# Kernel tuning notes

Measured on AMD Instinct MI355X. Metric: run time of the kernel, lower is better.

Reference implementation:

```python
import jax, jax.numpy as jnp
import numpy as np

DIM = 768
NUM_HEADS = 12
HIDDEN = int(DIM * 4.0)
EPS = 1e-5


def setup_inputs() -> dict:
    key = jax.random.key(0)
    ks = jax.random.split(key, 8)
    s = lambda k, shape, scale=0.02: jax.random.normal(k, shape, dtype=jnp.float32) * scale
    return {
        "x": jax.random.normal(ks[0], (8, 1024, DIM), dtype=jnp.float32),
        "ln1_g": jnp.ones((DIM,), jnp.float32),
        "ln1_b": jnp.zeros((DIM,), jnp.float32),
        "qkv_w": s(ks[1], (DIM, 3 * DIM)),
        "qkv_b": jnp.zeros((3 * DIM,), jnp.float32),
        "proj_w": s(ks[2], (DIM, DIM)),
        "proj_b": jnp.zeros((DIM,), jnp.float32),
        "ln2_g": jnp.ones((DIM,), jnp.float32),
        "ln2_b": jnp.zeros((DIM,), jnp.float32),
        "fc1_w": s(ks[3], (DIM, HIDDEN)),
        "fc1_b": jnp.zeros((HIDDEN,), jnp.float32),
        "fc2_w": s(ks[4], (HIDDEN, DIM)),
        "fc2_b": jnp.zeros((DIM,), jnp.float32),
    }


def layer_norm(x, g, b):
    mu = jnp.mean(x, axis=-1, keepdims=True)
    var = jnp.mean(jnp.square(x - mu), axis=-1, keepdims=True)
    return (x - mu) * jax.lax.rsqrt(var + EPS) * g + b


def reference(x, ln1_g, ln1_b, qkv_w, qkv_b, proj_w, proj_b,
              ln2_g, ln2_b, fc1_w, fc1_b, fc2_w, fc2_b):
    B, N, C = x.shape
    H = NUM_HEADS
    Dh = C // H
    scale = Dh ** -0.5

    # --- Attention (pre-norm) ---
    h = layer_norm(x, ln1_g, ln1_b)
    qkv = h @ qkv_w + qkv_b                       # [B, N, 3C]
    qkv = qkv.reshape(B, N, 3, H, Dh)
    q, k, v = qkv[:, :, 0], qkv[:, :, 1], qkv[:, :, 2]  # [B, N, H, Dh]
    attn = jnp.einsum("bqhd,bkhd->bhqk", q, k) * scale  # [B, H, N, N]
    attn = jax.nn.softmax(attn, axis=-1)
    o = jnp.einsum("bhqk,bkhd->bqhd", attn, v).reshape(B, N, C)
    x = x + (o @ proj_w + proj_b)

    # --- MLP (pre-norm) ---
    h = layer_norm(x, ln2_g, ln2_b)
    h = jax.nn.gelu(h @ fc1_w + fc1_b, approximate=False)  # torch nn.GELU = exact erf
    x = x + (h @ fc2_w + fc2_b)
    return x
```

## Files before the change

kernel.cpp:

```cpp
#include <hip/hip_runtime.h>
#include <hip/hip_bf16.h>
#include <cstdint>

using f32x4   = __attribute__((ext_vector_type(4))) float;
using f32x16  = __attribute__((ext_vector_type(16))) float;
using bf16x8  = __attribute__((ext_vector_type(8))) short;

__device__ inline ushort f2bf(float f) {
    union { float f; uint u; } x; x.f = f;
    uint u = x.u;
    return (ushort)((u + 0x7FFFu + ((u >> 16) & 1u)) >> 16);
}

__device__ inline void gload16(const ushort* g, ushort* lds) {
    __builtin_amdgcn_global_load_lds(
        (const __attribute__((address_space(1))) unsigned int*)g,
        (__attribute__((address_space(3))) unsigned int*)lds, 16, 0, 0);
}

__global__ __launch_bounds__(256) void transpose_cast(const float* __restrict__ w,
                                                      ushort* __restrict__ wt,
                                                      int K, int N) {
    __shared__ float tile[32][33];
    const int bn = blockIdx.x * 32;
    const int bk = blockIdx.y * 32;
    const int tx = threadIdx.x & 31, ty = threadIdx.x >> 5;
#pragma unroll
    for (int i = 0; i < 32; i += 8)
        tile[ty + i][tx] = w[(size_t)(bk + ty + i) * N + bn + tx];
    __syncthreads();
#pragma unroll
    for (int i = 0; i < 32; i += 8)
        wt[(size_t)(bn + ty + i) * K + bk + tx] = f2bf(tile[tx][ty + i]);
}

__global__ __launch_bounds__(256) void ln_bf16(const float* __restrict__ x,
                                               const float* __restrict__ g,
                                               const float* __restrict__ b,
                                               ushort* __restrict__ out) {
    const int row = blockIdx.x;
    const float* xr = x + (size_t)row * 768;
    const int t = threadIdx.x;
    float v0 = xr[t], v1 = xr[t + 256], v2 = xr[t + 512];
    float s  = v0 + v1 + v2;
    float sq = v0 * v0 + v1 * v1 + v2 * v2;
#pragma unroll
    for (int off = 32; off > 0; off >>= 1) {
        s  += __shfl_down(s, off);
        sq += __shfl_down(sq, off);
    }
    __shared__ float sa[4], sb[4];
    const int wv = t >> 6, lane = t & 63;
    if (lane == 0) { sa[wv] = s; sb[wv] = sq; }
    __syncthreads();
    s  = sa[0] + sa[1] + sa[2] + sa[3];
    sq = sb[0] + sb[1] + sb[2] + sb[3];
    const float mu   = s * (1.0f / 768.0f);
    const float var  = sq * (1.0f / 768.0f) - mu * mu;
    const float rstd = rsqrtf(var + 1e-5f);
    ushort* orow = out + (size_t)row * 768;
    orow[t]       = f2bf((v0 - mu) * rstd * g[t]       + b[t]);
    orow[t + 256] = f2bf((v1 - mu) * rstd * g[t + 256] + b[t + 256]);
    orow[t + 512] = f2bf((v2 - mu) * rstd * g[t + 512] + b[t + 512]);
}

template <int EPI, int SWZ>
__global__ __launch_bounds__(256) void gemm_bt(const ushort* __restrict__ A,
                                               const ushort* __restrict__ Bt,
                                               const float* __restrict__ bias,
                                               const float* __restrict__ resid,
                                               void* __restrict__ out,
                                               void* __restrict__ out2,
                                               int M, int N, int K, int gx) {
    __shared__ ushort As[3][128 * 32];
    __shared__ ushort Bs[3][128 * 32];
    int bm, bn;
    if (SWZ) {
        const int bid = blockIdx.x;
        const int x = bid & 7, s = bid >> 3;
        bm = ((s / gx) * 8 + x) * 128;
        bn = (s % gx) * 128;
    } else {
        bm = blockIdx.y * 128;
        bn = blockIdx.x * 128;
    }
    const int t    = threadIdx.x;
    const int lane = t & 63;
    const int w    = t >> 6;
    const int wr   = w >> 1, wc = w & 1;
    const int lr   = lane >> 4, lc = lane & 15;

    const f32x4 fzero = {0.f, 0.f, 0.f, 0.f};
    f32x4 acc[4][4];
#pragma unroll
    for (int ai = 0; ai < 4; ++ai)
#pragma unroll
        for (int bj = 0; bj < 4; ++bj) acc[ai][bj] = fzero;

    const int srow = lane >> 2;
    const int sk8  = (lane & 3) * 8;
    const ushort* Ag0 = A  + (size_t)(bm + w * 16 + srow) * K + sk8;
    const ushort* Ag1 = Ag0 + (size_t)64 * K;
    const ushort* Bg0 = Bt + (size_t)(bn + w * 16 + srow) * K + sk8;
    const ushort* Bg1 = Bg0 + (size_t)64 * K;
    const int lo0 = (w * 16) * 32, lo1 = (64 + w * 16) * 32;

    const int nt = K >> 5;
    auto issue = [&](int tile, int buf) {
        const int kb = tile << 5;
        gload16(Ag0 + kb, &As[buf][lo0]);
        gload16(Ag1 + kb, &As[buf][lo1]);
        gload16(Bg0 + kb, &Bs[buf][lo0]);
        gload16(Bg1 + kb, &Bs[buf][lo1]);
    };
    issue(0, 0);
    if (nt > 1) issue(1, 1);

    for (int tk = 0; tk < nt; ++tk) {
        if (tk + 1 < nt) asm volatile("s_waitcnt vmcnt(4)" ::: "memory");
        else             asm volatile("s_waitcnt vmcnt(0)" ::: "memory");
        __builtin_amdgcn_sched_barrier(0);
        __builtin_amdgcn_s_barrier();
        __builtin_amdgcn_sched_barrier(0);
        if (tk + 2 < nt) issue(tk + 2, (tk + 2) % 3);
        const int cb = tk % 3;
        bf16x8 af[4], bf[4];
#pragma unroll
        for (int ai = 0; ai < 4; ++ai)
            af[ai] = *(const bf16x8*)&As[cb][(wr * 64 + ai * 16 + lc) * 32 + lr * 8];
#pragma unroll
        for (int bj = 0; bj < 4; ++bj)
            bf[bj] = *(const bf16x8*)&Bs[cb][(wc * 64 + bj * 16 + lc) * 32 + lr * 8];
#pragma unroll
        for (int ai = 0; ai < 4; ++ai)
#pragma unroll
            for (int bj = 0; bj < 4; ++bj)
                acc[ai][bj] = __builtin_amdgcn_mfma_f32_16x16x32_bf16(af[ai], bf[bj],
                                                                      acc[ai][bj], 0, 0, 0);
    }

#pragma unroll
    for (int ai = 0; ai < 4; ++ai) {
#pragma unroll
        for (int bj = 0; bj < 4; ++bj) {
            int col  = bn + wc * 64 + bj * 16 + lc;
            float bs = bias[col];
            if (EPI == 3 && col >= 1536) {
                int row0 = bm + wr * 64 + ai * 16 + lr * 4;
                int bb   = row0 >> 10, key0 = row0 & 1023;
                int c    = col - 1536;
                int h    = c >> 6, d = c & 63;
                ushort4 pk;
                pk.x = f2bf(acc[ai][bj][0] + bs);
                pk.y = f2bf(acc[ai][bj][1] + bs);
                pk.z = f2bf(acc[ai][bj][2] + bs);
                pk.w = f2bf(acc[ai][bj][3] + bs);
                *(ushort4*)((ushort*)out2 +
                            ((size_t)(bb * 12 + h) * 64 + d) * 1024 + key0) = pk;
                continue;
            }
            const float qsc = (EPI == 3 && col < 768) ? 0.125f : 1.0f;
#pragma unroll
            for (int j = 0; j < 4; ++j) {
                int row   = bm + wr * 64 + ai * 16 + lr * 4 + j;
                float val = acc[ai][bj][j] + bs;
                if (EPI == 1) {
                    val += resid[(size_t)row * N + col];
                    ((float*)out)[(size_t)row * N + col] = val;
                } else if (EPI == 2) {
                    val = 0.5f * val * (1.0f + erff(val * 0.70710678118f));
                    ((ushort*)out)[(size_t)row * N + col] = f2bf(val);
                } else {
                    ((ushort*)out)[(size_t)row * N + col] = f2bf(val * qsc);
                }
            }
        }
    }
}

__global__ __launch_bounds__(256) void attn_mfma(const ushort* __restrict__ qkv,
                                                 const ushort* __restrict__ vT,
                                                 ushort* __restrict__ outb) {
    __shared__ ushort Kls[64 * 72];
    __shared__ ushort Vtls[64 * 72];

    const int bid = blockIdx.x;
    const int b   = bid / 96;
    const int rem = bid % 96;
    const int h   = rem >> 3;
    const int qc  = rem & 7;
    const int t    = threadIdx.x;
    const int w    = t >> 6;
    const int lane = t & 63;
    const int l31  = lane & 31;
    const int hi   = lane >> 5;
    const int q0   = qc * 128 + w * 32;
    const size_t bbase = (size_t)b * 1024;
    const ushort* vTh = vT + ((size_t)(b * 12 + h) * 64) * 1024;

    bf16x8 qb[4];
    {
        const size_t qrow = (bbase + q0 + l31) * 2304 + h * 64;
#pragma unroll
        for (int dblk = 0; dblk < 4; ++dblk)
            qb[dblk] = *(const bf16x8*)(qkv + qrow + dblk * 16 + hi * 8);
    }

    f32x16 O[2];
#pragma unroll
    for (int ob = 0; ob < 2; ++ob)
#pragma unroll
        for (int r = 0; r < 16; ++r) O[ob][r] = 0.0f;
    float l = 0.0f;

    for (int kt = 0; kt < 16; ++kt) {
        const int k0 = kt * 64;
        __syncthreads();
#pragma unroll
        for (int i = 0; i < 2; ++i) {
            int idx = t + i * 256;
            int key = idx >> 3, seg = idx & 7;
            uint4 u = *(const uint4*)(qkv + (bbase + k0 + key) * 2304 + 768 +
                                      h * 64 + seg * 8);
            *(uint4*)&Kls[key * 72 + seg * 8] = u;
        }
#pragma unroll
        for (int i = 0; i < 2; ++i) {
            int idx = t + i * 256;
            int d = idx >> 3, seg = idx & 7;
            uint4 u = *(const uint4*)(vTh + (size_t)d * 1024 + k0 + seg * 8);
            *(uint4*)&Vtls[d * 72 + seg * 8] = u;
        }
        __syncthreads();

        f32x16 s[2];
#pragma unroll
        for (int kb = 0; kb < 2; ++kb) {
            f32x16 acc;
#pragma unroll
            for (int r = 0; r < 16; ++r) acc[r] = 0.0f;
#pragma unroll
            for (int dblk = 0; dblk < 4; ++dblk) {
                bf16x8 ka = *(const bf16x8*)&Kls[(kb * 32 + l31) * 72 + dblk * 16 + hi * 8];
                acc = __builtin_amdgcn_mfma_f32_32x32x16_bf16(ka, qb[dblk], acc, 0, 0, 0);
            }
            s[kb] = acc;
        }

        float psum = 0.0f;
#pragma unroll
        for (int kb = 0; kb < 2; ++kb)
#pragma unroll
            for (int r = 0; r < 16; ++r) {
                float p = __expf(s[kb][r]);
                s[kb][r] = p;
                psum += p;
            }
        psum += __shfl_xor(psum, 32);
        l += psum;

        bf16x8 pb[4];
#pragma unroll
        for (int kb16 = 0; kb16 < 4; ++kb16) {
            const int sb = kb16 >> 1, r0 = (kb16 & 1) * 8;
            uint own01 = (uint)f2bf(s[sb][r0 + 0]) | ((uint)f2bf(s[sb][r0 + 1]) << 16);
            uint own23 = (uint)f2bf(s[sb][r0 + 2]) | ((uint)f2bf(s[sb][r0 + 3]) << 16);
            uint own45 = (uint)f2bf(s[sb][r0 + 4]) | ((uint)f2bf(s[sb][r0 + 5]) << 16);
            uint own67 = (uint)f2bf(s[sb][r0 + 6]) | ((uint)f2bf(s[sb][r0 + 7]) << 16);
            uint sw01 = __shfl_xor(own01, 32);
            uint sw23 = __shfl_xor(own23, 32);
            uint sw45 = __shfl_xor(own45, 32);
            uint sw67 = __shfl_xor(own67, 32);
            uint d0 = hi ? sw45 : own01;
            uint d1 = hi ? sw67 : own23;
            uint d2 = hi ? own45 : sw01;
            uint d3 = hi ? own67 : sw23;
            union { uint u[4]; bf16x8 v; } cvt;
            cvt.u[0] = d0; cvt.u[1] = d1; cvt.u[2] = d2; cvt.u[3] = d3;
            pb[kb16] = cvt.v;
        }

#pragma unroll
        for (int ob = 0; ob < 2; ++ob)
#pragma unroll
            for (int kb16 = 0; kb16 < 4; ++kb16) {
                bf16x8 va = *(const bf16x8*)&Vtls[(ob * 32 + l31) * 72 + kb16 * 16 + hi * 8];
                O[ob] = __builtin_amdgcn_mfma_f32_32x32x16_bf16(va, pb[kb16], O[ob], 0, 0, 0);
            }
    }

    const float inv = 1.0f / l;
    ushort* orow = outb + (bbase + q0 + l31) * 768 + h * 64;
#pragma unroll
    for (int ob = 0; ob < 2; ++ob)
#pragma unroll
        for (int qd = 0; qd < 4; ++qd) {
            ushort4 pk;
            pk.x = f2bf(O[ob][qd * 4 + 0] * inv);
            pk.y = f2bf(O[ob][qd * 4 + 1] * inv);
            pk.z = f2bf(O[ob][qd * 4 + 2] * inv);
            pk.w = f2bf(O[ob][qd * 4 + 3] * inv);
            *(ushort4*)(orow + ob * 32 + qd * 8 + hi * 4) = pk;
        }
}

extern "C" void kernel_launch(void* const* d_in, const int* in_sizes, int n_in,
                              void* d_out, int out_size, void* d_ws, size_t ws_size,
                              hipStream_t stream) {
    const float* x      = (const float*)d_in[0];
    const float* ln1_g  = (const float*)d_in[1];
    const float* ln1_b  = (const float*)d_in[2];
    const float* qkv_w  = (const float*)d_in[3];
    const float* qkv_b  = (const float*)d_in[4];
    const float* proj_w = (const float*)d_in[5];
    const float* proj_b = (const float*)d_in[6];
    const float* ln2_g  = (const float*)d_in[7];
    const float* ln2_b  = (const float*)d_in[8];
    const float* fc1_w  = (const float*)d_in[9];
    const float* fc1_b  = (const float*)d_in[10];
    const float* fc2_w  = (const float*)d_in[11];
    const float* fc2_b  = (const float*)d_in[12];

    char* ws = (char*)d_ws;
    auto alloc = [&](size_t bytes) {
        char* p = ws;
        ws += (bytes + 255) & ~(size_t)255;
        return p;
    };
    ushort* qkv_wt  = (ushort*)alloc((size_t)768 * 2304 * 2);
    ushort* proj_wt = (ushort*)alloc((size_t)768 * 768 * 2);
    ushort* fc1_wt  = (ushort*)alloc((size_t)768 * 3072 * 2);
    ushort* fc2_wt  = (ushort*)alloc((size_t)3072 * 768 * 2);
    ushort* hb      = (ushort*)alloc((size_t)8192 * 768 * 2);
    ushort* qkvb    = (ushort*)alloc((size_t)8192 * 2304 * 2);
    ushort* vTb     = (ushort*)alloc((size_t)96 * 64 * 1024 * 2);
    ushort* ob      = (ushort*)alloc((size_t)8192 * 768 * 2);
    float*  x1      = (float*)alloc((size_t)8192 * 768 * 4);
    ushort* h2b     = (ushort*)alloc((size_t)8192 * 768 * 2);
    ushort* h3b     = (ushort*)alloc((size_t)8192 * 3072 * 2);

    transpose_cast<<<dim3(2304 / 32, 768 / 32), 256, 0, stream>>>(qkv_w, qkv_wt, 768, 2304);
    transpose_cast<<<dim3(768 / 32, 768 / 32), 256, 0, stream>>>(proj_w, proj_wt, 768, 768);
    transpose_cast<<<dim3(3072 / 32, 768 / 32), 256, 0, stream>>>(fc1_w, fc1_wt, 768, 3072);
    transpose_cast<<<dim3(768 / 32, 3072 / 32), 256, 0, stream>>>(fc2_w, fc2_wt, 3072, 768);

    ln_bf16<<<8192, 256, 0, stream>>>(x, ln1_g, ln1_b, hb);
    gemm_bt<3, 1><<<18 * 64, 256, 0, stream>>>(
        hb, qkv_wt, qkv_b, nullptr, qkvb, vTb, 8192, 2304, 768, 18);
    attn_mfma<<<768, 256, 0, stream>>>(qkvb, vTb, ob);
    gemm_bt<1, 1><<<6 * 64, 256, 0, stream>>>(
        ob, proj_wt, proj_b, x, x1, nullptr, 8192, 768, 768, 6);
    ln_bf16<<<8192, 256, 0, stream>>>(x1, ln2_g, ln2_b, h2b);
    gemm_bt<2, 1><<<24 * 64, 256, 0, stream>>>(
        h2b, fc1_wt, fc1_b, nullptr, h3b, nullptr, 8192, 3072, 768, 24);
    gemm_bt<1, 1><<<6 * 64, 256, 0, stream>>>(
        h3b, fc2_wt, fc2_b, x1, (float*)d_out, nullptr, 8192, 768, 3072, 6);
}
```

Measured before the change: 297.1 us.

## Add wide 128x256-tile GEMM for QKV and FC1 projections

Introduces a gemm_bt_w kernel with a 128x256 block tile: each wave computes a 64x128 output with 4x8 MFMA accumulators and a triple-buffered LDS pipeline for A and B. The QKV and FC1 GEMMs (wide N) now use it, halving the block count and raising arithmetic intensity per A-tile load. The original gemm_bt epilogue is stripped of the GELU and QKV scatter paths, which move into the new kernel. The change raises register pressure (128 accumulator floats per thread) and LDS use, which may lower occupancy.

Measured after the change: 386.0 us. +29.9%, slower.

```diff
diff --git a/kernel.cpp b/kernel.cpp
--- a/kernel.cpp
+++ b/kernel.cpp
@@ -145,6 +145,106 @@
         for (int bj = 0; bj < 4; ++bj) {
             int col  = bn + wc * 64 + bj * 16 + lc;
             float bs = bias[col];
+#pragma unroll
+            for (int j = 0; j < 4; ++j) {
+                int row   = bm + wr * 64 + ai * 16 + lr * 4 + j;
+                float val = acc[ai][bj][j] + bs;
+                if (EPI == 1) {
+                    val += resid[(size_t)row * N + col];
+                    ((float*)out)[(size_t)row * N + col] = val;
+                } else {
+                    ((ushort*)out)[(size_t)row * N + col] = f2bf(val);
+                }
+            }
+        }
+    }
+}
+
+template <int EPI>
+__global__ __launch_bounds__(256) void gemm_bt_w(const ushort* __restrict__ A,
+                                                 const ushort* __restrict__ Bt,
+                                                 const float* __restrict__ bias,
+                                                 void* __restrict__ out,
+                                                 void* __restrict__ out2,
+                                                 int M, int N, int K, int gx) {
+    __shared__ ushort As[3][128 * 32];
+    __shared__ ushort Bs[3][256 * 32];
+    const int bid = blockIdx.x;
+    const int x = bid & 7, s = bid >> 3;
+    const int bm = ((s / gx) * 8 + x) * 128;
+    const int bn = (s % gx) * 256;
+    const int t    = threadIdx.x;
+    const int lane = t & 63;
+    const int w    = t >> 6;
+    const int wr   = w >> 1, wc = w & 1;
+    const int lr   = lane >> 4, lc = lane & 15;
+
+    const f32x4 fzero = {0.f, 0.f, 0.f, 0.f};
+    f32x4 acc[4][8];
+#pragma unroll
+    for (int ai = 0; ai < 4; ++ai)
+#pragma unroll
+        for (int bj = 0; bj < 8; ++bj) acc[ai][bj] = fzero;
+
+    const int srow = lane >> 2;
+    const int sk8  = (lane & 3) * 8;
+    const ushort* Ag0 = A + (size_t)(bm + w * 32 + srow) * K + sk8;
+    const ushort* Ag1 = Ag0 + (size_t)16 * K;
+    const ushort* Bg[4];
+#pragma unroll
+    for (int i = 0; i < 4; ++i)
+        Bg[i] = Bt + (size_t)(bn + w * 64 + 16 * i + srow) * K + sk8;
+    const int loA0 = (w * 32) * 32, loA1 = (w * 32 + 16) * 32;
+    int loB[4];
+#pragma unroll
+    for (int i = 0; i < 4; ++i) loB[i] = (w * 64 + 16 * i) * 32;
+
+    const int nt = K >> 5;
+    auto issue = [&](int tile, int buf) {
+        const int kb = tile << 5;
+        gload16(Ag0 + kb, &As[buf][loA0]);
+        gload16(Ag1 + kb, &As[buf][loA1]);
+#pragma unroll
+        for (int i = 0; i < 4; ++i)
+            gload16(Bg[i] + kb, &Bs[buf][loB[i]]);
+    };
+    issue(0, 0);
+    if (nt > 1) issue(1, 1);
+
+    for (int tk = 0; tk < nt; ++tk) {
+        if (tk + 1 < nt) asm volatile("s_waitcnt vmcnt(6)" ::: "memory");
+        else             asm volatile("s_waitcnt vmcnt(0)" ::: "memory");
+        __builtin_amdgcn_sched_barrier(0);
+        __builtin_amdgcn_s_barrier();
+        __builtin_amdgcn_sched_barrier(0);
+        if (tk + 2 < nt) issue(tk + 2, (tk + 2) % 3);
+        const int cb = tk % 3;
+        bf16x8 af[4];
+#pragma unroll
+        for (int ai = 0; ai < 4; ++ai)
+            af[ai] = *(const bf16x8*)&As[cb][(wr * 64 + ai * 16 + lc) * 32 + lr * 8];
+#pragma unroll
+        for (int g = 0; g < 2; ++g) {
+            bf16x8 bf[4];
+#pragma unroll
+            for (int j4 = 0; j4 < 4; ++j4)
+                bf[j4] = *(const bf16x8*)&Bs[cb][(wc * 128 + (g * 4 + j4) * 16 + lc) * 32 +
+                                                 lr * 8];
+#pragma unroll
+            for (int ai = 0; ai < 4; ++ai)
+#pragma unroll
+                for (int j4 = 0; j4 < 4; ++j4)
+                    acc[ai][g * 4 + j4] = __builtin_amdgcn_mfma_f32_16x16x32_bf16(
+                        af[ai], bf[j4], acc[ai][g * 4 + j4], 0, 0, 0);
+        }
+    }
+
+#pragma unroll
+    for (int ai = 0; ai < 4; ++ai) {
+#pragma unroll
+        for (int bj = 0; bj < 8; ++bj) {
+            int col  = bn + wc * 128 + bj * 16 + lc;
+            float bs = bias[col];
             if (EPI == 3 && col >= 1536) {
                 int row0 = bm + wr * 64 + ai * 16 + lr * 4;
                 int bb   = row0 >> 10, key0 = row0 & 1023;
@@ -164,10 +264,7 @@
             for (int j = 0; j < 4; ++j) {
                 int row   = bm + wr * 64 + ai * 16 + lr * 4 + j;
                 float val = acc[ai][bj][j] + bs;
-                if (EPI == 1) {
-                    val += resid[(size_t)row * N + col];
-                    ((float*)out)[(size_t)row * N + col] = val;
-                } else if (EPI == 2) {
+                if (EPI == 2) {
                     val = 0.5f * val * (1.0f + erff(val * 0.70710678118f));
                     ((ushort*)out)[(size_t)row * N + col] = f2bf(val);
                 } else {
@@ -345,14 +442,14 @@
     transpose_cast<<<dim3(768 / 32, 3072 / 32), 256, 0, stream>>>(fc2_w, fc2_wt, 3072, 768);
 
     ln_bf16<<<8192, 256, 0, stream>>>(x, ln1_g, ln1_b, hb);
-    gemm_bt<3, 1><<<18 * 64, 256, 0, stream>>>(
-        hb, qkv_wt, qkv_b, nullptr, qkvb, vTb, 8192, 2304, 768, 18);
+    gemm_bt_w<3><<<64 * 9, 256, 0, stream>>>(
+        hb, qkv_wt, qkv_b, qkvb, vTb, 8192, 2304, 768, 9);
     attn_mfma<<<768, 256, 0, stream>>>(qkvb, vTb, ob);
     gemm_bt<1, 1><<<6 * 64, 256, 0, stream>>>(
         ob, proj_wt, proj_b, x, x1, nullptr, 8192, 768, 768, 6);
     ln_bf16<<<8192, 256, 0, stream>>>(x1, ln2_g, ln2_b, h2b);
-    gemm_bt<2, 1><<<24 * 64, 256, 0, stream>>>(
-        h2b, fc1_wt, fc1_b, nullptr, h3b, nullptr, 8192, 3072, 768, 24);
+    gemm_bt_w<2><<<64 * 12, 256, 0, stream>>>(
+        h2b, fc1_wt, fc1_b, h3b, nullptr, 8192, 3072, 768, 12);
     gemm_bt<1, 1><<<6 * 64, 256, 0, stream>>>(
         h3b, fc2_wt, fc2_b, x1, (float*)d_out, nullptr, 8192, 768, 3072, 6);
 }
```
